# Kernel tuning notes

Hardware: AMD Instinct MI355X
Metric: run time of the kernel (lower is better)

## Reference

```python
import jax, jax.numpy as jnp
import numpy as np

B, S, D, H = 4, 2048, 1024, 4096  # batch, seq, d_model, mlp hidden
EPS = 1e-12  # F.normalize eps


def _linear(x, W, b):
    return x @ W.T + b


def setup_inputs() -> dict:
    key = jax.random.key(0)
    ks = jax.random.split(key, 14)
    s = lambda d: 1.0 / np.sqrt(d)
    return {
        "x": jax.random.normal(ks[0], (B, S, D), dtype=jnp.float32),
        "Wq": jax.random.normal(ks[1], (D, D), dtype=jnp.float32) * s(D),
        "bq": jax.random.normal(ks[2], (D,), dtype=jnp.float32) * 0.01,
        "Wk": jax.random.normal(ks[3], (D, D), dtype=jnp.float32) * s(D),
        "bk": jax.random.normal(ks[4], (D,), dtype=jnp.float32) * 0.01,
        "Wv": jax.random.normal(ks[5], (D, D), dtype=jnp.float32) * s(D),
        "bv": jax.random.normal(ks[6], (D,), dtype=jnp.float32) * 0.01,
        "W1": jax.random.normal(ks[7], (D, D), dtype=jnp.float32) * s(D),
        "b1": jax.random.normal(ks[8], (D,), dtype=jnp.float32) * 0.01,
        "W2": jax.random.normal(ks[9], (H, D), dtype=jnp.float32) * s(D),
        "b2": jax.random.normal(ks[10], (H,), dtype=jnp.float32) * 0.01,
        "W3": jax.random.normal(ks[11], (D, H), dtype=jnp.float32) * s(H),
        "b3": jax.random.normal(ks[12], (D,), dtype=jnp.float32) * 0.01,
    }


def reference(x, Wq, bq, Wk, bk, Wv, bv, W1, b1, W2, b2, W3, b3):
    Q = _linear(x, Wq, bq)  # [B,S,D]
    K = _linear(x, Wk, bk)
    V = _linear(x, Wv, bv)
    # L2-normalize along feature dim (F.normalize, p=2, dim=2)
    Q = Q / jnp.maximum(jnp.linalg.norm(Q, axis=2, keepdims=True), EPS)
    K = K / jnp.maximum(jnp.linalg.norm(K, axis=2, keepdims=True), EPS)
    sim = jnp.einsum("bqd,bkd->bqk", Q, K)  # cosine similarities [B,S,S]
    attn = jax.nn.softmax(sim, axis=2)
    out = jnp.einsum("bqk,bkd->bqd", attn, V)  # [B,S,D]
    # MLP: Linear->relu->Linear->relu->Linear (dropout identity in eval)
    h = jax.nn.relu(_linear(out, W1, b1))
    h = jax.nn.relu(_linear(h, W2, b2))
    return _linear(h, W3, b3)
```

## Files before the change

kernel.cpp:

```cpp
#include <hip/hip_runtime.h>


using u16 = unsigned short;
using bf16x8 = __attribute__((ext_vector_type(8))) __bf16;
using f32x4  = __attribute__((ext_vector_type(4))) float;

__device__ __forceinline__ u16 f2bf(float f) {
  unsigned u = __float_as_uint(f);
  unsigned r = (u + 0x7FFFu + ((u >> 16) & 1u)) >> 16;
  return (u16)r;
}

__global__ __launch_bounds__(256) void cast_bf16_kernel(
    const float* __restrict__ in, u16* __restrict__ out, int n4) {
  int i = blockIdx.x * 256 + threadIdx.x;
  if (i < n4) {
    float4 v = reinterpret_cast<const float4*>(in)[i];
    ushort4 o;
    o.x = f2bf(v.x); o.y = f2bf(v.y); o.z = f2bf(v.z); o.w = f2bf(v.w);
    reinterpret_cast<ushort4*>(out)[i] = o;
  }
}

__global__ __launch_bounds__(256) void l2norm_kernel(
    const float* __restrict__ in, u16* __restrict__ out) {
  __shared__ float red[4];
  long row = blockIdx.x;
  const int tid = threadIdx.x, lane = tid & 63, wave = tid >> 6;
  const float* p = in + row * 1024;
  float4 x = *reinterpret_cast<const float4*>(p + tid * 4);
  float ss = x.x * x.x + x.y * x.y + x.z * x.z + x.w * x.w;
#pragma unroll
  for (int o = 32; o; o >>= 1) ss += __shfl_xor(ss, o);
  if (lane == 0) red[wave] = ss;
  __syncthreads();
  ss = red[0] + red[1] + red[2] + red[3];
  float s = 1.0f / fmaxf(sqrtf(ss), 1e-12f);
  ushort4 o;
  o.x = f2bf(x.x * s); o.y = f2bf(x.y * s); o.z = f2bf(x.z * s); o.w = f2bf(x.w * s);
  *reinterpret_cast<ushort4*>(out + row * 1024 + tid * 4) = o;
}

__global__ void transpose_kernel(const u16* __restrict__ in, u16* __restrict__ out,
                                 int rows, int cols) {
  __shared__ u16 t[32][33];
  const int c0 = blockIdx.x * 32, r0 = blockIdx.y * 32;
  const long off = (long)blockIdx.z * rows * cols;
  const u16* ib = in + off;
  u16* ob = out + off;
  const int tx = threadIdx.x, ty = threadIdx.y;
#pragma unroll
  for (int j = 0; j < 4; ++j)
    t[ty + j * 8][tx] = ib[(long)(r0 + ty + j * 8) * cols + c0 + tx];
  __syncthreads();
#pragma unroll
  for (int j = 0; j < 4; ++j)
    ob[(long)(c0 + ty + j * 8) * rows + r0 + tx] = t[tx][ty + j * 8];
}

__global__ __launch_bounds__(256) void softmax_kernel(
    const float* __restrict__ in, u16* __restrict__ out) {
  __shared__ float red[4];
  long row = blockIdx.x;
  const int tid = threadIdx.x, lane = tid & 63, wave = tid >> 6;
  const float* p = in + row * 2048;
  float v[8];
  float4 a = *reinterpret_cast<const float4*>(p + tid * 8);
  float4 b = *reinterpret_cast<const float4*>(p + tid * 8 + 4);
  v[0] = a.x; v[1] = a.y; v[2] = a.z; v[3] = a.w;
  v[4] = b.x; v[5] = b.y; v[6] = b.z; v[7] = b.w;
  float m = v[0];
#pragma unroll
  for (int i = 1; i < 8; ++i) m = fmaxf(m, v[i]);
#pragma unroll
  for (int o = 32; o; o >>= 1) m = fmaxf(m, __shfl_xor(m, o));
  if (lane == 0) red[wave] = m;
  __syncthreads();
  m = fmaxf(fmaxf(red[0], red[1]), fmaxf(red[2], red[3]));
  float s = 0.0f;
#pragma unroll
  for (int i = 0; i < 8; ++i) { v[i] = __expf(v[i] - m); s += v[i]; }
#pragma unroll
  for (int o = 32; o; o >>= 1) s += __shfl_xor(s, o);
  __syncthreads();
  if (lane == 0) red[wave] = s;
  __syncthreads();
  s = red[0] + red[1] + red[2] + red[3];
  float inv = 1.0f / s;
  ushort4 o0, o1;
  o0.x = f2bf(v[0] * inv); o0.y = f2bf(v[1] * inv);
  o0.z = f2bf(v[2] * inv); o0.w = f2bf(v[3] * inv);
  o1.x = f2bf(v[4] * inv); o1.y = f2bf(v[5] * inv);
  o1.z = f2bf(v[6] * inv); o1.w = f2bf(v[7] * inv);
  *reinterpret_cast<ushort4*>(out + row * 2048 + tid * 8) = o0;
  *reinterpret_cast<ushort4*>(out + row * 2048 + tid * 8 + 4) = o1;
}

template <int BM, int DEPTH, int MODE>
__global__ __launch_bounds__(512, 2) void gemm8p(
    const u16* __restrict__ A, const u16* __restrict__ Bw,
    const float* __restrict__ bias, void* __restrict__ Cout,
    const float* __restrict__ bias2, void* __restrict__ Cout2,
    const float* __restrict__ bias3, void* __restrict__ Cout3,
    int N, int K, long batchA, long batchB, long batchC, int relu,
    int gx, int gy) {
  static_assert(MODE != 2 || BM == 256, "QKV route assumes BM=256");
  constexpr int MF  = BM / 32;
  constexpr int MH  = MF / 2;
  constexpr int ASZ = BM * 64;
  constexpr int BSZ = 256 * 64;
  constexpr int AR  = BM / 64;
  __shared__ u16 lds[DEPTH * (ASZ + BSZ)];
  u16* const ldsA = lds;
  u16* const ldsB = lds + DEPTH * ASZ;

  const int nwg = gridDim.x;
  const int lid = blockIdx.x;
  const int q = nwg >> 3, r = nwg & 7;
  const int xcd = lid & 7, jj = lid >> 3;
  const int wg = (xcd < r ? xcd * (q + 1) : r * (q + 1) + (xcd - r) * q) + jj;
  const int bx = wg % gx;
  const int rest = wg / gx;
  const int by = rest % gy;
  const int bz = rest / gy;

  const int tid = threadIdx.x, wave = tid >> 6, lane = tid & 63;
  const int wr = wave >> 2, wc = wave & 3;
  const int fr = lane & 15, hi = lane >> 4;

  const long Abase = bz * batchA + (long)by * BM * K;
  const long Bbase = bz * batchB + (long)bx * 256 * K;

  int aoff[MF][2], boff[4][2];
#pragma unroll
  for (int m = 0; m < MF; ++m) {
    const int qm = m / MH, ml = m % MH;
    const int row = qm * (BM / 2) + wr * (BM / 4) + ml * 16 + fr;
#pragma unroll
    for (int ks = 0; ks < 2; ++ks) {
      const int gg = ks * 4 + hi;
      aoff[m][ks] = row * 64 + ((gg ^ (row & 7)) * 8);
    }
  }
#pragma unroll
  for (int n = 0; n < 4; ++n) {
    const int qn = n >> 1, nl = n & 1;
    const int row = qn * 128 + wc * 32 + nl * 16 + fr;
#pragma unroll
    for (int ks = 0; ks < 2; ++ks) {
      const int gg = ks * 4 + hi;
      boff[n][ks] = row * 64 + ((gg ^ (row & 7)) * 8);
    }
  }

  const int rA = wave * 8 + (lane >> 3);
  const int g8 = (((lane & 7) ^ (lane >> 3)) * 8);
  long asrc[AR], bsrc[4];
#pragma unroll
  for (int rr = 0; rr < AR; ++rr) asrc[rr] = Abase + (long)(rr * 64 + rA) * K + g8;
#pragma unroll
  for (int rr = 0; rr < 4; ++rr) bsrc[rr] = Bbase + (long)(rr * 64 + rA) * K + g8;

#define STAGE_A(bufp, rr, k0)                                                  \
  __builtin_amdgcn_global_load_lds(                                            \
      (const __attribute__((address_space(1))) void*)(A + asrc[rr] + (k0)),    \
      (__attribute__((address_space(3))) void*)((bufp) + (rr) * 4096 + wave * 512), \
      16, 0, 0)
#define STAGE_B(bufp, rr, k0)                                                  \
  __builtin_amdgcn_global_load_lds(                                            \
      (const __attribute__((address_space(1))) void*)(Bw + bsrc[rr] + (k0)),   \
      (__attribute__((address_space(3))) void*)((bufp) + (rr) * 4096 + wave * 512), \
      16, 0, 0)

  const int NT = K >> 6;

  if constexpr (DEPTH == 2) {
#pragma unroll
    for (int rr = 0; rr < AR; ++rr) STAGE_A(ldsA, rr, 0);
#pragma unroll
    for (int rr = 0; rr < 4; ++rr) STAGE_B(ldsB, rr, 0);
    asm volatile("s_waitcnt vmcnt(0)" ::: "memory");
  } else {
#pragma unroll
    for (int rr = 0; rr < AR; ++rr) STAGE_A(ldsA, rr, 0);
#pragma unroll
    for (int rr = 0; rr < 4; ++rr) STAGE_B(ldsB, rr, 0);
    if (NT > 1) {
#pragma unroll
      for (int rr = 0; rr < AR; ++rr) STAGE_A(ldsA + ASZ, rr, 64);
#pragma unroll
      for (int rr = 0; rr < 4; ++rr) STAGE_B(ldsB + BSZ, rr, 64);
      asm volatile("s_waitcnt vmcnt(6)" ::: "memory");
    } else {
      asm volatile("s_waitcnt vmcnt(0)" ::: "memory");
    }
  }
  __builtin_amdgcn_s_barrier();

  f32x4 acc[MF][4] = {};

#define READ_AHALF(dst, h)                                                     \
  _Pragma("unroll") for (int mm = 0; mm < MH; ++mm)                            \
  _Pragma("unroll") for (int ks = 0; ks < 2; ++ks)                             \
    dst[mm][ks] = *reinterpret_cast<const bf16x8*>(&curA[aoff[(h) * MH + mm][ks]]);
#define READ_BHALF(dst, h)                                                     \
  _Pragma("unroll") for (int nn = 0; nn < 2; ++nn)                             \
  _Pragma("unroll") for (int ks = 0; ks < 2; ++ks)                             \
    dst[nn][ks] = *reinterpret_cast<const bf16x8*>(&curB[boff[(h) * 2 + nn][ks]]);
#define MFMA_Q(ah, bh, qm, qn)                                                 \
  __builtin_amdgcn_s_setprio(1);                                               \
  _Pragma("unroll") for (int ks = 0; ks < 2; ++ks)                             \
  _Pragma("unroll") for (int mm = 0; mm < MH; ++mm)                            \
  _Pragma("unroll") for (int nn = 0; nn < 2; ++nn)                             \
    acc[(qm) * MH + mm][(qn) * 2 + nn] =                                       \
        __builtin_amdgcn_mfma_f32_16x16x32_bf16(                               \
            ah[mm][ks], bh[nn][ks], acc[(qm) * MH + mm][(qn) * 2 + nn], 0, 0, 0); \
  __builtin_amdgcn_s_setprio(0);

  for (int t = 0; t < NT; ++t) {
    u16* curA = ldsA + (t % DEPTH) * ASZ;
    u16* curB = ldsB + (t % DEPTH) * BSZ;
    const int ts = t + DEPTH - 1;
    const bool st = ts < NT;
    u16* nxtA = ldsA + (ts % DEPTH) * ASZ;
    u16* nxtB = ldsB + (ts % DEPTH) * BSZ;
    const int k0n = ts << 6;

    bf16x8 a0[MH][2], a1[MH][2], b0[2][2], b1[2][2];

    READ_AHALF(a0, 0)
    READ_BHALF(b0, 0)
    if (st) {
#pragma unroll
      for (int rr = 0; rr < AR / 2; ++rr) STAGE_A(nxtA, rr, k0n);
    }
    __builtin_amdgcn_s_barrier();
    MFMA_Q(a0, b0, 0, 0)
    if constexpr (DEPTH == 2) {
      if (st) asm volatile("s_waitcnt vmcnt(2)" ::: "memory");
      else    asm volatile("s_waitcnt vmcnt(0)" ::: "memory");
    }
    __builtin_amdgcn_s_barrier();

    READ_BHALF(b1, 1)
    if (st) {
#pragma unroll
      for (int rr = AR / 2; rr < AR; ++rr) STAGE_A(nxtA, rr, k0n);
    }
    __builtin_amdgcn_s_barrier();
    MFMA_Q(a0, b1, 0, 1)
    __builtin_amdgcn_s_barrier();

    READ_AHALF(a1, 1)
    if (st) { STAGE_B(nxtB, 0, k0n); STAGE_B(nxtB, 1, k0n); }
    __builtin_amdgcn_s_barrier();
    MFMA_Q(a1, b0, 1, 0)
    __builtin_amdgcn_s_barrier();

    if (st) { STAGE_B(nxtB, 2, k0n); STAGE_B(nxtB, 3, k0n); }
    __builtin_amdgcn_s_barrier();
    MFMA_Q(a1, b1, 1, 1)
    if constexpr (DEPTH == 2) {
      if (st) asm volatile("s_waitcnt vmcnt(2)" ::: "memory");
    } else {
      if (st) asm volatile("s_waitcnt vmcnt(6)" ::: "memory");
      else    asm volatile("s_waitcnt vmcnt(0)" ::: "memory");
    }
    __builtin_amdgcn_s_barrier();
  }
#undef STAGE_A
#undef STAGE_B
#undef READ_AHALF
#undef READ_BHALF
#undef MFMA_Q

  const long cbase = bz * batchC;
  const int crow = by * BM;
  int ccol = bx * 256;
  const float* bp = bias;
  void* cp = Cout;
  bool obf = (MODE == 1);
  int Nst = N;
  if constexpr (MODE == 2) {
    const int sel = ccol >> 10;
    if (sel == 1) { bp = bias2; cp = Cout2; }
    else if (sel == 2) { bp = bias3; cp = Cout3; obf = true; }
    ccol &= 1023;
    Nst = 1024;
  }
#pragma unroll
  for (int m = 0; m < MF; ++m) {
    const int qm = m / MH, ml = m % MH;
    const int r0 = crow + qm * (BM / 2) + wr * (BM / 4) + ml * 16 + hi * 4;
#pragma unroll
    for (int n = 0; n < 4; ++n) {
      const int qn = n >> 1, nl = n & 1;
      const int c = ccol + qn * 128 + wc * 32 + nl * 16 + fr;
      const float bb = bp ? bp[c] : 0.0f;
#pragma unroll
      for (int j = 0; j < 4; ++j) {
        float v = acc[m][n][j] + bb;
        if (relu) v = fmaxf(v, 0.0f);
        const long idx = cbase + (long)(r0 + j) * Nst + c;
        if (obf) ((u16*)cp)[idx] = f2bf(v);
        else     ((float*)cp)[idx] = v;
      }
    }
  }
}

extern "C" void kernel_launch(void* const* d_in, const int* in_sizes, int n_in,
                              void* d_out, int out_size, void* d_ws, size_t ws_size,
                              hipStream_t stream) {
  (void)in_sizes; (void)n_in; (void)out_size; (void)ws_size;
  const float* x  = (const float*)d_in[0];
  const float* Wq = (const float*)d_in[1];
  const float* bq = (const float*)d_in[2];
  const float* Wk = (const float*)d_in[3];
  const float* bk = (const float*)d_in[4];
  const float* Wv = (const float*)d_in[5];
  const float* bv = (const float*)d_in[6];
  const float* W1 = (const float*)d_in[7];
  const float* b1 = (const float*)d_in[8];
  const float* W2 = (const float*)d_in[9];
  const float* b2 = (const float*)d_in[10];
  const float* W3 = (const float*)d_in[11];
  const float* b3 = (const float*)d_in[12];

  char* ws = (char*)d_ws;
  const size_t MB = 1u << 20;
  float* Qf   = (float*)(ws + 0);
  float* Kf   = Qf + (size_t)8192 * 1024;
  float* simf = (float*)(ws + 0);
  u16*   h2   = (u16*)(ws + 0);
  u16* xbf = (u16*)(ws + 64 * MB);
  u16* Vbf = xbf + (size_t)8192 * 1024;
  u16* P   = (u16*)(ws + 64 * MB);
  u16* Wq_b = (u16*)(ws + 96 * MB);
  u16* Wk_b = Wq_b + 1048576;
  u16* Wv_b = Wk_b + 1048576;
  u16* W1_b = Wv_b + 1048576;
  u16* W2_b = W1_b + 1048576;
  u16* W3_b = W2_b + 4194304;
  u16* Qn = (u16*)(ws + 120 * MB);
  u16* Kn = Qn + 8388608;
  u16* Vt = Kn + 8388608;
  u16* attnout = Qn;
  u16* h1      = Kn;

  cast_bf16_kernel<<<8192, 256, 0, stream>>>(x,  xbf,  2097152);
  cast_bf16_kernel<<<1024, 256, 0, stream>>>(Wq, Wq_b, 262144);
  cast_bf16_kernel<<<1024, 256, 0, stream>>>(Wk, Wk_b, 262144);
  cast_bf16_kernel<<<1024, 256, 0, stream>>>(Wv, Wv_b, 262144);
  cast_bf16_kernel<<<1024, 256, 0, stream>>>(W1, W1_b, 262144);
  cast_bf16_kernel<<<4096, 256, 0, stream>>>(W2, W2_b, 1048576);
  cast_bf16_kernel<<<4096, 256, 0, stream>>>(W3, W3_b, 1048576);

  gemm8p<256, 2, 2><<<dim3(12 * 32), 512, 0, stream>>>(
      xbf, Wq_b, bq, Qf, bk, Kf, bv, Vbf, 3072, 1024, 0, 0, 0, 0, 12, 32);
  l2norm_kernel<<<8192, 256, 0, stream>>>(Qf, Qn);
  l2norm_kernel<<<8192, 256, 0, stream>>>(Kf, Kn);
  transpose_kernel<<<dim3(32, 64, 4), dim3(32, 8), 0, stream>>>(Vbf, Vt, 2048, 1024);
  gemm8p<256, 2, 0><<<dim3(8 * 8 * 4), 512, 0, stream>>>(
      Qn, Kn, nullptr, simf, nullptr, nullptr, nullptr, nullptr,
      2048, 1024, 2097152L, 2097152L, 4194304L, 0, 8, 8);
  softmax_kernel<<<8192, 256, 0, stream>>>(simf, P);
  gemm8p<128, 3, 1><<<dim3(4 * 16 * 4), 512, 0, stream>>>(
      P, Vt, nullptr, attnout, nullptr, nullptr, nullptr, nullptr,
      1024, 2048, 4194304L, 2097152L, 2097152L, 0, 4, 16);
  gemm8p<128, 3, 1><<<dim3(4 * 64), 512, 0, stream>>>(
      attnout, W1_b, b1, h1, nullptr, nullptr, nullptr, nullptr,
      1024, 1024, 0, 0, 0, 1, 4, 64);
  gemm8p<256, 2, 1><<<dim3(16 * 32), 512, 0, stream>>>(
      h1, W2_b, b2, h2, nullptr, nullptr, nullptr, nullptr,
      4096, 1024, 0, 0, 0, 1, 16, 32);
  gemm8p<128, 3, 0><<<dim3(4 * 64), 512, 0, stream>>>(
      h2, W3_b, b3, (float*)d_out, nullptr, nullptr, nullptr, nullptr,
      1024, 4096, 0, 0, 0, 0, 4, 64);
}
```

Baseline: 403.7 us.

## Fuse cast launches, emit bf16 Q/K from QKV GEMM, retile QKV to BM=128

The seven separate fp32-to-bf16 cast launches become one segmented multi-cast kernel, which removes launch overhead and tail gaps between launches. The QKV projection GEMM now writes Q and K as bf16 instead of fp32, and the L2-norm kernels read bf16. This halves the intermediate write and read traffic. The QKV GEMM also switches to a 128-row tile with depth 3, doubling the grid for better occupancy. Rounding Q and K to bf16 before normalization adds a little precision loss.

```diff
diff --git a/kernel.cpp b/kernel.cpp
--- a/kernel.cpp
+++ b/kernel.cpp
@@ -10,26 +10,36 @@
   unsigned r = (u + 0x7FFFu + ((u >> 16) & 1u)) >> 16;
   return (u16)r;
 }
-
-__global__ __launch_bounds__(256) void cast_bf16_kernel(
-    const float* __restrict__ in, u16* __restrict__ out, int n4) {
-  int i = blockIdx.x * 256 + threadIdx.x;
-  if (i < n4) {
-    float4 v = reinterpret_cast<const float4*>(in)[i];
-    ushort4 o;
-    o.x = f2bf(v.x); o.y = f2bf(v.y); o.z = f2bf(v.z); o.w = f2bf(v.w);
-    reinterpret_cast<ushort4*>(out)[i] = o;
-  }
+__device__ __forceinline__ float bf2f(u16 h) {
+  return __uint_as_float(((unsigned)h) << 16);
+}
+
+struct CastSegs {
+  const float* src[7];
+  u16* dst[7];
+  long beg[8];
+};
+__global__ __launch_bounds__(256) void cast_multi_kernel(CastSegs cs) {
+  long idx = (long)blockIdx.x * 256 + threadIdx.x;
+  if (idx >= cs.beg[7]) return;
+  int seg = 0;
+#pragma unroll
+  for (int s = 1; s < 7; ++s) seg += (idx >= cs.beg[s]) ? 1 : 0;
+  const long loc = idx - cs.beg[seg];
+  float4 v = reinterpret_cast<const float4*>(cs.src[seg])[loc];
+  ushort4 o;
+  o.x = f2bf(v.x); o.y = f2bf(v.y); o.z = f2bf(v.z); o.w = f2bf(v.w);
+  reinterpret_cast<ushort4*>(cs.dst[seg])[loc] = o;
 }
 
 __global__ __launch_bounds__(256) void l2norm_kernel(
-    const float* __restrict__ in, u16* __restrict__ out) {
+    const u16* __restrict__ in, u16* __restrict__ out) {
   __shared__ float red[4];
   long row = blockIdx.x;
   const int tid = threadIdx.x, lane = tid & 63, wave = tid >> 6;
-  const float* p = in + row * 1024;
-  float4 x = *reinterpret_cast<const float4*>(p + tid * 4);
-  float ss = x.x * x.x + x.y * x.y + x.z * x.z + x.w * x.w;
+  ushort4 h = *reinterpret_cast<const ushort4*>(in + row * 1024 + tid * 4);
+  float x0 = bf2f(h.x), x1 = bf2f(h.y), x2 = bf2f(h.z), x3 = bf2f(h.w);
+  float ss = x0 * x0 + x1 * x1 + x2 * x2 + x3 * x3;
 #pragma unroll
   for (int o = 32; o; o >>= 1) ss += __shfl_xor(ss, o);
   if (lane == 0) red[wave] = ss;
@@ -37,7 +47,7 @@
   ss = red[0] + red[1] + red[2] + red[3];
   float s = 1.0f / fmaxf(sqrtf(ss), 1e-12f);
   ushort4 o;
-  o.x = f2bf(x.x * s); o.y = f2bf(x.y * s); o.z = f2bf(x.z * s); o.w = f2bf(x.w * s);
+  o.x = f2bf(x0 * s); o.y = f2bf(x1 * s); o.z = f2bf(x2 * s); o.w = f2bf(x3 * s);
   *reinterpret_cast<ushort4*>(out + row * 1024 + tid * 4) = o;
 }
 
@@ -104,7 +114,6 @@
     const float* __restrict__ bias3, void* __restrict__ Cout3,
     int N, int K, long batchA, long batchB, long batchC, int relu,
     int gx, int gy) {
-  static_assert(MODE != 2 || BM == 256, "QKV route assumes BM=256");
   constexpr int MF  = BM / 32;
   constexpr int MH  = MF / 2;
   constexpr int ASZ = BM * 64;
@@ -279,12 +288,12 @@
   int ccol = bx * 256;
   const float* bp = bias;
   void* cp = Cout;
-  bool obf = (MODE == 1);
+  bool obf = (MODE == 1) || (MODE == 2);
   int Nst = N;
   if constexpr (MODE == 2) {
     const int sel = ccol >> 10;
     if (sel == 1) { bp = bias2; cp = Cout2; }
-    else if (sel == 2) { bp = bias3; cp = Cout3; obf = true; }
+    else if (sel == 2) { bp = bias3; cp = Cout3; }
     ccol &= 1023;
     Nst = 1024;
   }
@@ -329,8 +338,8 @@
 
   char* ws = (char*)d_ws;
   const size_t MB = 1u << 20;
-  float* Qf   = (float*)(ws + 0);
-  float* Kf   = Qf + (size_t)8192 * 1024;
+  u16* Qbf  = (u16*)(ws + 0);
+  u16* Kbf  = Qbf + 8388608;
   float* simf = (float*)(ws + 0);
   u16*   h2   = (u16*)(ws + 0);
   u16* xbf = (u16*)(ws + 64 * MB);
@@ -348,18 +357,24 @@
   u16* attnout = Qn;
   u16* h1      = Kn;
 
-  cast_bf16_kernel<<<8192, 256, 0, stream>>>(x,  xbf,  2097152);
-  cast_bf16_kernel<<<1024, 256, 0, stream>>>(Wq, Wq_b, 262144);
-  cast_bf16_kernel<<<1024, 256, 0, stream>>>(Wk, Wk_b, 262144);
-  cast_bf16_kernel<<<1024, 256, 0, stream>>>(Wv, Wv_b, 262144);
-  cast_bf16_kernel<<<1024, 256, 0, stream>>>(W1, W1_b, 262144);
-  cast_bf16_kernel<<<4096, 256, 0, stream>>>(W2, W2_b, 1048576);
-  cast_bf16_kernel<<<4096, 256, 0, stream>>>(W3, W3_b, 1048576);
-
-  gemm8p<256, 2, 2><<<dim3(12 * 32), 512, 0, stream>>>(
-      xbf, Wq_b, bq, Qf, bk, Kf, bv, Vbf, 3072, 1024, 0, 0, 0, 0, 12, 32);
-  l2norm_kernel<<<8192, 256, 0, stream>>>(Qf, Qn);
-  l2norm_kernel<<<8192, 256, 0, stream>>>(Kf, Kn);
+  CastSegs cs;
+  cs.src[0] = x;  cs.dst[0] = xbf;
+  cs.src[1] = Wq; cs.dst[1] = Wq_b;
+  cs.src[2] = Wk; cs.dst[2] = Wk_b;
+  cs.src[3] = Wv; cs.dst[3] = Wv_b;
+  cs.src[4] = W1; cs.dst[4] = W1_b;
+  cs.src[5] = W2; cs.dst[5] = W2_b;
+  cs.src[6] = W3; cs.dst[6] = W3_b;
+  long szs[7] = {2097152, 262144, 262144, 262144, 262144, 1048576, 1048576};
+  long acc0 = 0;
+  for (int i = 0; i < 7; ++i) { cs.beg[i] = acc0; acc0 += szs[i]; }
+  cs.beg[7] = acc0;
+  cast_multi_kernel<<<dim3((unsigned)((acc0 + 255) / 256)), 256, 0, stream>>>(cs);
+
+  gemm8p<128, 3, 2><<<dim3(12 * 64), 512, 0, stream>>>(
+      xbf, Wq_b, bq, Qbf, bk, Kbf, bv, Vbf, 3072, 1024, 0, 0, 0, 0, 12, 64);
+  l2norm_kernel<<<8192, 256, 0, stream>>>(Qbf, Qn);
+  l2norm_kernel<<<8192, 256, 0, stream>>>(Kbf, Kn);
   transpose_kernel<<<dim3(32, 64, 4), dim3(32, 8), 0, stream>>>(Vbf, Vt, 2048, 1024);
   gemm8p<256, 2, 0><<<dim3(8 * 8 * 4), 512, 0, stream>>>(
       Qn, Kn, nullptr, simf, nullptr, nullptr, nullptr, nullptr,
```

After: 393.4 us. 2.5% less time.
